# Performance work log

Measured on AMD Instinct MI355X. Metric: run time of the kernel, lower is better.

The kernel has to match this reference:

```python
import jax, jax.numpy as jnp
import numpy as np


def setup_inputs() -> dict:
    key = jax.random.key(0)
    k1, k2 = jax.random.split(key)
    B, T, D = 32, 512, 512
    x = jax.random.normal(k1, (B, T, D), dtype=jnp.float32)
    duration = jax.random.randint(k2, (B, T), 0, 8, dtype=jnp.int32)
    return {"x": x, "duration": duration, "max_len": 2048}


def reference(x, duration, max_len):
    """Vectorized length regulator.

    x:        [B, T, D] float
    duration: [B, T] int frames per phoneme
    max_len:  static python int, padded output length

    Returns (output [B, max_len, D], mel_lengths [B]).
    Frame t of sample b copies phoneme j where j is the first index with
    cumsum(duration)[b, j] > t (i.e. searchsorted right). Frames beyond the
    total duration are zero-padded; sequences longer than max_len are truncated
    (mel_lengths reports the untruncated length, matching the torch module,
    with the all-zero-duration edge case yielding length 1).
    """
    B, T, D = x.shape
    csum = jnp.cumsum(duration, axis=1)            # [B, T]
    dur_sum = csum[:, -1]                          # [B]
    t = jnp.arange(max_len, dtype=csum.dtype)      # [max_len]
    # phoneme index for each output frame: searchsorted(csum[b], t, 'right')
    idx = jax.vmap(lambda c: jnp.searchsorted(c, t, side='right'))(csum)  # [B, max_len]
    idx = jnp.clip(idx, 0, T - 1)
    out = jnp.take_along_axis(x, idx[:, :, None], axis=1)  # [B, max_len, D]
    valid = t[None, :] < dur_sum[:, None]                  # [B, max_len]
    out = jnp.where(valid[:, :, None], out, jnp.zeros((), dtype=x.dtype))
    mel_lengths = jnp.maximum(dur_sum, 1).astype(jnp.int32)
    return out, mel_lengths
```

## Files before the change

### kernel.cpp

```cpp
#include <hip/hip_runtime.h>


#define BB      32
#define TT      512
#define DD      512
#define MAXLEN  2048
#define RPF     (DD / 4)
#define GTH     (1 << 19)
#define NSWEEP  16

typedef float f4 __attribute__((ext_vector_type(4)));

__global__ __launch_bounds__(512) void lr_scan_kernel(
    const int* __restrict__ dur, int* __restrict__ idxt,
    float* __restrict__ mel_out) {
  __shared__ int wsum[8];
  const int b    = blockIdx.x;
  const int tid  = threadIdx.x;
  const int lane = tid & 63;
  const int wid  = tid >> 6;

  const int d = dur[b * TT + tid];
  int v = d;
#pragma unroll
  for (int off = 1; off < 64; off <<= 1) {
    int n = __shfl_up(v, off, 64);
    if (lane >= off) v += n;
  }
  if (lane == 63) wsum[wid] = v;
  __syncthreads();

  int woff = 0, dsum = 0;
#pragma unroll
  for (int i = 0; i < 8; ++i) {
    int w = wsum[i];
    dsum += w;
    if (i < wid) woff += w;
  }
  v += woff;

  if (tid == 0) mel_out[b] = (float)(dsum > 1 ? dsum : 1);

  int start = v - d;
  int end   = v;
  if (start > MAXLEN) start = MAXLEN;
  if (end   > MAXLEN) end   = MAXLEN;
  int* row = idxt + b * MAXLEN;
  for (int t = start; t < end; ++t) row[t] = tid;
  for (int t = dsum + tid; t < MAXLEN; t += TT) row[t] = -1;
}

__global__ __launch_bounds__(256) void lr_sweep_kernel(
    const int* __restrict__ idxt, const f4* __restrict__ x,
    f4* __restrict__ out) {
  const int g  = blockIdx.x * 256 + threadIdx.x;
  const int d4 = g & (RPF - 1);
  const int t  = (g >> 7) & (MAXLEN - 1);
  const int hi = g >> 18;
  const f4 zero = {0.f, 0.f, 0.f, 0.f};

#pragma unroll
  for (int h = 0; h < 2; ++h) {
    int idxv[8];
#pragma unroll
    for (int k = 0; k < 8; ++k) {
      const int b = 2 * (h * 8 + k) + hi;
      idxv[k] = idxt[b * MAXLEN + t];
    }
#pragma unroll
    for (int k = 0; k < 8; ++k) {
      const int kk = h * 8 + k;
      const int b  = 2 * kk + hi;
      const int idx = idxv[k];
      f4 v = zero;
      if (idx >= 0) {
        v = x[((size_t)b * TT + idx) * RPF + d4];
      }
      out[(size_t)g + (size_t)kk * GTH] = v;
    }
  }
}

extern "C" void kernel_launch(void* const* d_in, const int* in_sizes, int n_in,
                              void* d_out, int out_size, void* d_ws, size_t ws_size,
                              hipStream_t stream) {
  const float* x   = (const float*)d_in[0];
  const int*   dur = (const int*)d_in[1];
  float* out = (float*)d_out;
  float* mel_out = out + (size_t)BB * MAXLEN * DD;
  int* idxt = (int*)d_ws;

  lr_scan_kernel<<<BB, 512, 0, stream>>>(dur, idxt, mel_out);
  lr_sweep_kernel<<<GTH / 256, 256, 0, stream>>>(idxt, (const f4*)x, (f4*)out);
}
```

Measured before the change: 168.8 us.

## Replace batch-interleaved sweep with persistent grid-stride copy kernel

The gather/copy kernel now launches a fixed grid of 512 blocks that stride linearly across the whole output, batching eight loads ahead of eight stores per iteration, in place of the 2048-block launch where each thread handled sixteen batches at a fixed frame and column. Output writes become contiguous per step and there are fewer, longer-lived blocks. The aim is to cut launch and tail overhead and to keep more memory requests in flight. The cost is 64-bit address arithmetic and fewer blocks, which could leave the device's compute units underfilled.

```diff
diff --git a/kernel.cpp b/kernel.cpp
--- a/kernel.cpp
+++ b/kernel.cpp
@@ -6,8 +6,10 @@
 #define DD      512
 #define MAXLEN  2048
 #define RPF     (DD / 4)
-#define GTH     (1 << 19)
-#define NSWEEP  16
+#define NF4     (BB * MAXLEN * RPF)
+#define CBLK    512
+#define CTH     (CBLK * 256)
+#define STEPS   (NF4 / CTH)
 
 typedef float f4 __attribute__((ext_vector_type(4)));
 
@@ -50,33 +52,33 @@
   for (int t = dsum + tid; t < MAXLEN; t += TT) row[t] = -1;
 }
 
-__global__ __launch_bounds__(256) void lr_sweep_kernel(
+__global__ __launch_bounds__(256) void lr_copy_kernel(
     const int* __restrict__ idxt, const f4* __restrict__ x,
     f4* __restrict__ out) {
-  const int g  = blockIdx.x * 256 + threadIdx.x;
-  const int d4 = g & (RPF - 1);
-  const int t  = (g >> 7) & (MAXLEN - 1);
-  const int hi = g >> 18;
+  const int g = blockIdx.x * 256 + threadIdx.x;
   const f4 zero = {0.f, 0.f, 0.f, 0.f};
 
+  for (int s = 0; s < STEPS; s += 8) {
+    int idx[8];
 #pragma unroll
-  for (int h = 0; h < 2; ++h) {
-    int idxv[8];
+    for (int u = 0; u < 8; ++u) {
+      const size_t e = (size_t)g + (size_t)(s + u) * CTH;
+      idx[u] = idxt[e >> 7];
+    }
+    f4 v[8];
 #pragma unroll
-    for (int k = 0; k < 8; ++k) {
-      const int b = 2 * (h * 8 + k) + hi;
-      idxv[k] = idxt[b * MAXLEN + t];
+    for (int u = 0; u < 8; ++u) {
+      const size_t e = (size_t)g + (size_t)(s + u) * CTH;
+      v[u] = zero;
+      if (idx[u] >= 0) {
+        const size_t b = e >> 18;
+        v[u] = x[(b * TT + (size_t)idx[u]) * RPF + (e & (RPF - 1))];
+      }
     }
 #pragma unroll
-    for (int k = 0; k < 8; ++k) {
-      const int kk = h * 8 + k;
-      const int b  = 2 * kk + hi;
-      const int idx = idxv[k];
-      f4 v = zero;
-      if (idx >= 0) {
-        v = x[((size_t)b * TT + idx) * RPF + d4];
-      }
-      out[(size_t)g + (size_t)kk * GTH] = v;
+    for (int u = 0; u < 8; ++u) {
+      const size_t e = (size_t)g + (size_t)(s + u) * CTH;
+      out[e] = v[u];
     }
   }
 }
@@ -91,5 +93,5 @@
   int* idxt = (int*)d_ws;
 
   lr_scan_kernel<<<BB, 512, 0, stream>>>(dur, idxt, mel_out);
-  lr_sweep_kernel<<<GTH / 256, 256, 0, stream>>>(idxt, (const f4*)x, (f4*)out);
+  lr_copy_kernel<<<CBLK, 256, 0, stream>>>(idxt, (const f4*)x, (f4*)out);
 }
```

Result: no change. 169.1 us (+0.1%).
